# Optimization experiments

Hardware: AMD Instinct MI355X
Metric: run time of the kernel (lower is better)

## Reference

```python
import jax, jax.numpy as jnp
import numpy as np

N_NODES = 50000
N_EDGES = 800000
IN_CH = 128
OUT_CH = 64
HID_CH = 2 * OUT_CH  # 128


def gcn_conv(x, edge_index, W, b, n_nodes):
    """PyG GCNConv: linear -> add self-loops -> sym-normalized scatter-add -> bias."""
    h = x @ W  # [N, out]
    loop = jnp.arange(n_nodes)
    row = jnp.concatenate([edge_index[0], loop])  # source nodes
    col = jnp.concatenate([edge_index[1], loop])  # target nodes
    deg = jax.ops.segment_sum(jnp.ones_like(col, dtype=h.dtype), col, num_segments=n_nodes)
    dinv = jnp.where(deg > 0, jax.lax.rsqrt(jnp.maximum(deg, 1.0)), 0.0)
    norm = dinv[row] * dinv[col]  # [E+N]
    msg = h[row] * norm[:, None]  # gather + scale, [E+N, out]
    out = jax.ops.segment_sum(msg, col, num_segments=n_nodes)  # scatter-add
    return out + b


def setup_inputs() -> dict:
    key = jax.random.key(0)
    ks = jax.random.split(key, 9)
    x = jax.random.normal(ks[0], (N_NODES, IN_CH), dtype=jnp.float32)
    edge_index = jax.random.randint(ks[1], (2, N_EDGES), 0, N_NODES, dtype=jnp.int64)
    s_in = 1.0 / np.sqrt(IN_CH)
    s_hid = 1.0 / np.sqrt(HID_CH)
    W1 = jax.random.normal(ks[2], (IN_CH, HID_CH), dtype=jnp.float32) * s_in
    b1 = jnp.zeros((HID_CH,), dtype=jnp.float32)
    W2 = jax.random.normal(ks[3], (HID_CH, OUT_CH), dtype=jnp.float32) * s_hid
    b2 = jnp.zeros((OUT_CH,), dtype=jnp.float32)
    W3 = jax.random.normal(ks[4], (HID_CH, OUT_CH), dtype=jnp.float32) * s_hid
    b3 = jnp.zeros((OUT_CH,), dtype=jnp.float32)
    return {"x": x, "edge_index": edge_index, "W1": W1, "b1": b1,
            "W2": W2, "b2": b2, "W3": W3, "b3": b3}


def reference(x, edge_index, W1, b1, W2, b2, W3, b3):
    act = jax.nn.relu
    hidden = act(gcn_conv(x, edge_index, W1, b1, N_NODES))
    x1 = act(gcn_conv(hidden, edge_index, W2, b2, N_NODES))
    x2 = act(gcn_conv(hidden, edge_index, W3, b3, N_NODES))
    return (x1, x2)
```

## Files before the change

### kernel.cpp

```cpp
#include <hip/hip_runtime.h>

#define N_NODES 50000
#define N_EDGES 800000
#define CH 128
#define WT_PAD 136
#define DUMMY N_NODES
#define SLOT_LOG 6
#define AGG_HALF_BLKS 1563
#define PREP_THREADS (128 * 256)

typedef __attribute__((ext_vector_type(8))) short short8;
typedef __attribute__((ext_vector_type(4))) float floatx4;

__device__ __forceinline__ short f2bf(float f) {
    union { float f; unsigned u; } v; v.f = f;
    unsigned r = v.u + 0x7fff + ((v.u >> 16) & 1);
    return (short)(r >> 16);
}
__device__ __forceinline__ float bflo(unsigned u) {
    union { unsigned u; float f; } v; v.u = u << 16; return v.f;
}
__device__ __forceinline__ float bfhi(unsigned u) {
    union { unsigned u; float f; } v; v.u = u & 0xffff0000u; return v.f;
}


__global__ __launch_bounds__(256) void prep_kernel(const float* __restrict__ W1,
                                                   const float* __restrict__ W2,
                                                   const float* __restrict__ W3,
                                                   const float* __restrict__ b2,
                                                   const float* __restrict__ b3,
                                                   unsigned short* __restrict__ Wt1,
                                                   unsigned short* __restrict__ Wt23,
                                                   float* __restrict__ b23,
                                                   int* __restrict__ counts,
                                                   unsigned short* __restrict__ sorted_src,
                                                   unsigned int* __restrict__ gdummy) {
    int i = blockIdx.x * blockDim.x + threadIdx.x;
    if (i < 128 * 128) {
        int n = i >> 7, k = i & 127;
        Wt1[i] = (unsigned short)f2bf(W1[k * 128 + n]);
        float w = (n < 64) ? W2[k * 64 + n] : W3[k * 64 + (n - 64)];
        Wt23[i] = (unsigned short)f2bf(w);
    } else if (i < 128 * 128 + 128) {
        int k2 = i - 128 * 128;
        b23[k2] = (k2 < 64) ? b2[k2] : b3[k2 - 64];
    } else if (i < 128 * 128 + 192) {
        gdummy[i - (128 * 128 + 128)] = 0;
    }
    for (int j = i; j < N_NODES; j += PREP_THREADS) counts[j] = 0;
    const unsigned dpat = ((unsigned)DUMMY) | (((unsigned)DUMMY) << 16);
    uint4 dfill = make_uint4(dpat, dpat, dpat, dpat);
    uint4* sp = (uint4*)sorted_src;
    for (int j = i; j < (N_NODES << SLOT_LOG) / 8; j += PREP_THREADS) sp[j] = dfill;
}


__global__ void rank_scatter(const int* __restrict__ ei, int* __restrict__ counts,
                             unsigned short* __restrict__ sorted_src) {
    int e = blockIdx.x * blockDim.x + threadIdx.x;
    if (e < N_EDGES) {
        int src = __builtin_nontemporal_load(ei + e);
        int dst = __builtin_nontemporal_load(ei + N_EDGES + e);
        int r = atomicAdd(&counts[dst], 1);
        if (r < 64) sorted_src[(dst << SLOT_LOG) + r] = (unsigned short)src;
    }
}


template <bool A_BF16>
__global__ __launch_bounds__(256) void gemm_mfma(const void* __restrict__ Ain,
                                                 const unsigned short* __restrict__ Wt,
                                                 const int* __restrict__ degs,
                                                 unsigned short* __restrict__ g) {
    __shared__ unsigned short lds[128 * WT_PAD];
    int tid = threadIdx.x;
    int wave = tid >> 6, lane = tid & 63;
    int quad = lane >> 4, ln = lane & 15;

    {
        int r = tid >> 1, h = tid & 1;
        const int4* src = (const int4*)(Wt + r * 128 + h * 64);
#pragma unroll
        for (int i = 0; i < 8; ++i)
            *(int4*)&lds[r * WT_PAD + h * 64 + i * 8] = src[i];
    }

    int row_base = blockIdx.x * 64 + wave * 16;
    int arow = row_base + ln;
    bool ok = arow < N_NODES;
    short8 afrag[4];
    if (A_BF16) {
        const unsigned short* A = (const unsigned short*)Ain;
#pragma unroll
        for (int kk = 0; kk < 4; ++kk) {
            short8 v = {};
            if (ok) v = *(const short8*)(A + arow * 128 + kk * 32 + quad * 8);
            afrag[kk] = v;
        }
    } else {
        const float* A = (const float*)Ain;
#pragma unroll
        for (int kk = 0; kk < 4; ++kk) {
            short8 v = {};
            if (ok) {
                const floatx4* p = (const floatx4*)(A + arow * 128 + kk * 32 + quad * 8);
                floatx4 fa = p[0], fb = p[1];
                v[0] = f2bf(fa.x); v[1] = f2bf(fa.y); v[2] = f2bf(fa.z); v[3] = f2bf(fa.w);
                v[4] = f2bf(fb.x); v[5] = f2bf(fb.y); v[6] = f2bf(fb.z); v[7] = f2bf(fb.w);
            }
            afrag[kk] = v;
        }
    }
    __syncthreads();

    floatx4 acc[8] = {};
#pragma unroll
    for (int n0 = 0; n0 < 8; ++n0) {
#pragma unroll
        for (int kk = 0; kk < 4; ++kk) {
            short8 b = *(const short8*)&lds[(n0 * 16 + ln) * WT_PAD + kk * 32 + quad * 8];
            acc[n0] = __builtin_amdgcn_mfma_f32_16x16x32_bf16(afrag[kk], b, acc[n0], 0, 0, 0);
        }
    }

    __syncthreads();
    unsigned short* st = &lds[wave * 16 * WT_PAD];
    float dv[4];
#pragma unroll
    for (int r = 0; r < 4; ++r) {
        int node = row_base + quad * 4 + r;
        dv[r] = (node < N_NODES) ? rsqrtf((float)(degs[node] + 1)) : 0.f;
    }
#pragma unroll
    for (int n0 = 0; n0 < 8; ++n0)
#pragma unroll
        for (int r = 0; r < 4; ++r)
            st[(quad * 4 + r) * WT_PAD + n0 * 16 + ln] =
                (unsigned short)f2bf(acc[n0][r] * dv[r]);
    __syncthreads();

#pragma unroll
    for (int i = 0; i < 4; ++i) {
        int row = i * 4 + quad;
        int node = row_base + row;
        short8 v = *(const short8*)&st[row * WT_PAD + ln * 8];
        if (node < N_NODES) *(short8*)(g + node * 128 + ln * 8) = v;
    }
}


template <int MODE>
__global__ __launch_bounds__(256) void aggregate_bf16(const unsigned short* __restrict__ g,
                                                      const int* __restrict__ degs,
                                                      const unsigned short* __restrict__ srcs,
                                                      const float* __restrict__ bias,
                                                      void* __restrict__ outp) {
    int h = 0, nb = blockIdx.x;
    if (nb >= AGG_HALF_BLKS) { h = 1; nb -= AGG_HALF_BLKS; }
    int n = nb * 32 + (threadIdx.x >> 3);
    if (n >= N_NODES) return;
    int c4 = threadIdx.x & 7;
    int hoff = h * 8;
    const uint4* grow = (const uint4*)g;
    uint4 u = grow[n * 16 + hoff + c4];
    float a0 = bflo(u.x), a1 = bfhi(u.x), a2 = bflo(u.y), a3 = bfhi(u.y);
    float a4 = bflo(u.z), a5 = bfhi(u.z), a6 = bflo(u.w), a7 = bfhi(u.w);
    float c0 = 0.f, c1 = 0.f, c2 = 0.f, c3 = 0.f, c5 = 0.f, c6 = 0.f, c7 = 0.f, c8 = 0.f;
    int deg = degs[n];
    int beg = n << SLOT_LOG;
    int pend = beg + ((deg + 3) & ~3);
    int e = beg;
    for (; e + 8 <= pend; e += 8) {
        ushort4 sa = *(const ushort4*)&srcs[e];
        ushort4 sb = *(const ushort4*)&srcs[e + 4];
        uint4 v0 = grow[sa.x * 16 + hoff + c4];
        uint4 v1 = grow[sa.y * 16 + hoff + c4];
        uint4 v2 = grow[sa.z * 16 + hoff + c4];
        uint4 v3 = grow[sa.w * 16 + hoff + c4];
        uint4 v4 = grow[sb.x * 16 + hoff + c4];
        uint4 v5 = grow[sb.y * 16 + hoff + c4];
        uint4 v6 = grow[sb.z * 16 + hoff + c4];
        uint4 v7 = grow[sb.w * 16 + hoff + c4];
        a0 += bflo(v0.x); a1 += bfhi(v0.x); a2 += bflo(v0.y); a3 += bfhi(v0.y);
        a4 += bflo(v0.z); a5 += bfhi(v0.z); a6 += bflo(v0.w); a7 += bfhi(v0.w);
        c0 += bflo(v1.x); c1 += bfhi(v1.x); c2 += bflo(v1.y); c3 += bfhi(v1.y);
        c5 += bflo(v1.z); c6 += bfhi(v1.z); c7 += bflo(v1.w); c8 += bfhi(v1.w);
        a0 += bflo(v2.x); a1 += bfhi(v2.x); a2 += bflo(v2.y); a3 += bfhi(v2.y);
        a4 += bflo(v2.z); a5 += bfhi(v2.z); a6 += bflo(v2.w); a7 += bfhi(v2.w);
        c0 += bflo(v3.x); c1 += bfhi(v3.x); c2 += bflo(v3.y); c3 += bfhi(v3.y);
        c5 += bflo(v3.z); c6 += bfhi(v3.z); c7 += bflo(v3.w); c8 += bfhi(v3.w);
        a0 += bflo(v4.x); a1 += bfhi(v4.x); a2 += bflo(v4.y); a3 += bfhi(v4.y);
        a4 += bflo(v4.z); a5 += bfhi(v4.z); a6 += bflo(v4.w); a7 += bfhi(v4.w);
        c0 += bflo(v5.x); c1 += bfhi(v5.x); c2 += bflo(v5.y); c3 += bfhi(v5.y);
        c5 += bflo(v5.z); c6 += bfhi(v5.z); c7 += bflo(v5.w); c8 += bfhi(v5.w);
        a0 += bflo(v6.x); a1 += bfhi(v6.x); a2 += bflo(v6.y); a3 += bfhi(v6.y);
        a4 += bflo(v6.z); a5 += bfhi(v6.z); a6 += bflo(v6.w); a7 += bfhi(v6.w);
        c0 += bflo(v7.x); c1 += bfhi(v7.x); c2 += bflo(v7.y); c3 += bfhi(v7.y);
        c5 += bflo(v7.z); c6 += bfhi(v7.z); c7 += bflo(v7.w); c8 += bfhi(v7.w);
    }
    if (e < pend) {
        ushort4 sa = *(const ushort4*)&srcs[e];
        uint4 v0 = grow[sa.x * 16 + hoff + c4];
        uint4 v1 = grow[sa.y * 16 + hoff + c4];
        uint4 v2 = grow[sa.z * 16 + hoff + c4];
        uint4 v3 = grow[sa.w * 16 + hoff + c4];
        a0 += bflo(v0.x); a1 += bfhi(v0.x); a2 += bflo(v0.y); a3 += bfhi(v0.y);
        a4 += bflo(v0.z); a5 += bfhi(v0.z); a6 += bflo(v0.w); a7 += bfhi(v0.w);
        c0 += bflo(v1.x); c1 += bfhi(v1.x); c2 += bflo(v1.y); c3 += bfhi(v1.y);
        c5 += bflo(v1.z); c6 += bfhi(v1.z); c7 += bflo(v1.w); c8 += bfhi(v1.w);
        a0 += bflo(v2.x); a1 += bfhi(v2.x); a2 += bflo(v2.y); a3 += bfhi(v2.y);
        a4 += bflo(v2.z); a5 += bfhi(v2.z); a6 += bflo(v2.w); a7 += bfhi(v2.w);
        c0 += bflo(v3.x); c1 += bfhi(v3.x); c2 += bflo(v3.y); c3 += bfhi(v3.y);
        c5 += bflo(v3.z); c6 += bfhi(v3.z); c7 += bflo(v3.w); c8 += bfhi(v3.w);
    }
    a0 += c0; a1 += c1; a2 += c2; a3 += c3; a4 += c5; a5 += c6; a6 += c7; a7 += c8;
    float d = rsqrtf((float)(deg + 1));
    float4 bv0 = ((const float4*)bias)[h * 16 + c4 * 2];
    float4 bv1 = ((const float4*)bias)[h * 16 + c4 * 2 + 1];
    float o0 = fmaxf(d * a0 + bv0.x, 0.f);
    float o1 = fmaxf(d * a1 + bv0.y, 0.f);
    float o2 = fmaxf(d * a2 + bv0.z, 0.f);
    float o3 = fmaxf(d * a3 + bv0.w, 0.f);
    float o4 = fmaxf(d * a4 + bv1.x, 0.f);
    float o5 = fmaxf(d * a5 + bv1.y, 0.f);
    float o6 = fmaxf(d * a6 + bv1.z, 0.f);
    float o7 = fmaxf(d * a7 + bv1.w, 0.f);
    if (MODE == 0) {
        uint4 w;
        w.x = ((unsigned)(unsigned short)f2bf(o0)) | (((unsigned)(unsigned short)f2bf(o1)) << 16);
        w.y = ((unsigned)(unsigned short)f2bf(o2)) | (((unsigned)(unsigned short)f2bf(o3)) << 16);
        w.z = ((unsigned)(unsigned short)f2bf(o4)) | (((unsigned)(unsigned short)f2bf(o5)) << 16);
        w.w = ((unsigned)(unsigned short)f2bf(o6)) | (((unsigned)(unsigned short)f2bf(o7)) << 16);
        ((uint4*)outp)[n * 16 + hoff + c4] = w;
    } else {
        float* out = (float*)outp + (size_t)h * N_NODES * 64;
        floatx4* o = (floatx4*)out + n * 16 + c4 * 2;
        floatx4 w0; w0.x = o0; w0.y = o1; w0.z = o2; w0.w = o3;
        floatx4 w1; w1.x = o4; w1.y = o5; w1.z = o6; w1.w = o7;
        __builtin_nontemporal_store(w0, o);
        __builtin_nontemporal_store(w1, o + 1);
    }
}


extern "C" void kernel_launch(void* const* d_in, const int* in_sizes, int n_in,
                              void* d_out, int out_size, void* d_ws, size_t ws_size,
                              hipStream_t stream) {
    const float* x  = (const float*)d_in[0];
    const int*   ei = (const int*)d_in[1];
    const float* W1 = (const float*)d_in[2];
    const float* b1 = (const float*)d_in[3];
    const float* W2 = (const float*)d_in[4];
    const float* b2 = (const float*)d_in[5];
    const float* W3 = (const float*)d_in[6];
    const float* b3 = (const float*)d_in[7];
    float* out = (float*)d_out;

    char* w = (char*)d_ws;
    int*            counts     = (int*)(w + 0);
    unsigned short* sorted_src = (unsigned short*)(w + 3686400);
    unsigned short* Wt1        = (unsigned short*)(w + 10485760);
    unsigned short* Wt23       = (unsigned short*)(w + 10518528);
    float*          b23        = (float*)(w + 10551296);
    unsigned short* g1         = (unsigned short*)(w + 12582912);
    unsigned short* hidden     = (unsigned short*)(w + 25690112);

    prep_kernel<<<128, 256, 0, stream>>>(W1, W2, W3, b2, b3, Wt1, Wt23, b23, counts,
                                         sorted_src, (unsigned int*)(g1 + N_NODES * 128));
    rank_scatter<<<(N_EDGES + 255) / 256, 256, 0, stream>>>(ei, counts, sorted_src);

    const int gemm_blocks = (N_NODES + 63) / 64;
    const int agg_blocks = 2 * AGG_HALF_BLKS;

    gemm_mfma<false><<<gemm_blocks, 256, 0, stream>>>(x, Wt1, counts, g1);
    aggregate_bf16<0><<<agg_blocks, 256, 0, stream>>>(g1, counts, sorted_src, b1, hidden);

    gemm_mfma<true><<<gemm_blocks, 256, 0, stream>>>(hidden, Wt23, counts, g1);
    aggregate_bf16<1><<<agg_blocks, 256, 0, stream>>>(g1, counts, sorted_src, b23, out);
}
```

Before: 209.3 us.

## Replace global atomic edge scatter with two-pass bucketed partition and LDS CSR build

Graph preprocessing is rebuilt. Edges are first bucketed by destination into groups of 128 nodes using block-local histograms and scans, then each bucket builds its fixed-slot adjacency in shared memory and writes it out with coalesced stores. This replaces per-edge global atomics on node counters, scattered 2-byte global writes, and the full global dummy-fill of sorted_src. In exchange it adds one extra kernel and an intermediate buffer, buckets are capped at 3072 edges, and the aggregation now clamps degree to 64.

```diff
diff --git a/kernel.cpp b/kernel.cpp
--- a/kernel.cpp
+++ b/kernel.cpp
@@ -7,7 +7,11 @@
 #define DUMMY N_NODES
 #define SLOT_LOG 6
 #define AGG_HALF_BLKS 1563
-#define PREP_THREADS (128 * 256)
+
+#define NBUCK 391
+#define BUCK_CAP 3072
+#define EPB 4096
+#define PART_BLOCKS 196
 
 typedef __attribute__((ext_vector_type(8))) short short8;
 typedef __attribute__((ext_vector_type(4))) float floatx4;
@@ -33,8 +37,7 @@
                                                    unsigned short* __restrict__ Wt1,
                                                    unsigned short* __restrict__ Wt23,
                                                    float* __restrict__ b23,
-                                                   int* __restrict__ counts,
-                                                   unsigned short* __restrict__ sorted_src,
+                                                   int* __restrict__ bucket_cnt,
                                                    unsigned int* __restrict__ gdummy) {
     int i = blockIdx.x * blockDim.x + threadIdx.x;
     if (i < 128 * 128) {
@@ -48,22 +51,95 @@
     } else if (i < 128 * 128 + 192) {
         gdummy[i - (128 * 128 + 128)] = 0;
     }
-    for (int j = i; j < N_NODES; j += PREP_THREADS) counts[j] = 0;
+    if (i < NBUCK) bucket_cnt[i] = 0;
+}
+
+
+__global__ __launch_bounds__(256) void partition(const int* __restrict__ ei,
+                                                 int* __restrict__ bucket_cnt,
+                                                 unsigned* __restrict__ bucket_data) {
+    __shared__ int hcnt[512], hscan[512], htmp[512];
+    __shared__ int s_shift[512];
+    __shared__ unsigned stg[EPB];
+    __shared__ int dsti[EPB];
+    int tid = threadIdx.x;
+    int e0 = blockIdx.x * EPB;
+
+    for (int i = tid; i < 512; i += 256) hcnt[i] = 0;
+    __syncthreads();
+    for (int j = tid; j < EPB; j += 256) {
+        int e = e0 + j;
+        if (e < N_EDGES) atomicAdd(&hcnt[ei[N_EDGES + e] >> 7], 1);
+    }
+    __syncthreads();
+    for (int i = tid; i < 512; i += 256) hscan[i] = hcnt[i];
+    __syncthreads();
+    for (int off = 1; off < 512; off <<= 1) {
+        for (int i = tid; i < 512; i += 256) htmp[i] = hscan[i] + (i >= off ? hscan[i - off] : 0);
+        __syncthreads();
+        for (int i = tid; i < 512; i += 256) hscan[i] = htmp[i];
+        __syncthreads();
+    }
+    for (int b = tid; b < NBUCK; b += 256) {
+        int c = hcnt[b];
+        int excl = hscan[b] - c;
+        int g = (c > 0) ? atomicAdd(&bucket_cnt[b], c) : 0;
+        s_shift[b] = g - excl;
+        htmp[b] = excl;
+    }
+    __syncthreads();
+    for (int j = tid; j < EPB; j += 256) {
+        int e = e0 + j;
+        if (e < N_EDGES) {
+            int src = ei[e];
+            int d = ei[N_EDGES + e];
+            int b = d >> 7;
+            int pos = atomicAdd(&htmp[b], 1);
+            stg[pos] = ((unsigned)(d & 127) << 16) | (unsigned)src;
+            int gidx = s_shift[b] + pos;
+            dsti[pos] = (gidx < BUCK_CAP) ? (b * BUCK_CAP + gidx) : -1;
+        }
+    }
+    __syncthreads();
+    int tot = N_EDGES - e0; if (tot > EPB) tot = EPB;
+    for (int j = tid; j < tot; j += 256) {
+        int di = dsti[j];
+        if (di >= 0) bucket_data[di] = stg[j];
+    }
+}
+
+
+__global__ __launch_bounds__(256) void csr_build(const unsigned* __restrict__ bucket_data,
+                                                 const int* __restrict__ bucket_cnt,
+                                                 int* __restrict__ counts,
+                                                 unsigned short* __restrict__ sorted_src) {
+    __shared__ uint4 slots4[1024];
+    __shared__ int ctr[128];
+    unsigned short* slots = (unsigned short*)slots4;
+    int tid = threadIdx.x, b = blockIdx.x;
+
+    for (int i = tid; i < 128; i += 256) ctr[i] = 0;
     const unsigned dpat = ((unsigned)DUMMY) | (((unsigned)DUMMY) << 16);
-    uint4 dfill = make_uint4(dpat, dpat, dpat, dpat);
-    uint4* sp = (uint4*)sorted_src;
-    for (int j = i; j < (N_NODES << SLOT_LOG) / 8; j += PREP_THREADS) sp[j] = dfill;
-}
-
-
-__global__ void rank_scatter(const int* __restrict__ ei, int* __restrict__ counts,
-                             unsigned short* __restrict__ sorted_src) {
-    int e = blockIdx.x * blockDim.x + threadIdx.x;
-    if (e < N_EDGES) {
-        int src = __builtin_nontemporal_load(ei + e);
-        int dst = __builtin_nontemporal_load(ei + N_EDGES + e);
-        int r = atomicAdd(&counts[dst], 1);
-        if (r < 64) sorted_src[(dst << SLOT_LOG) + r] = (unsigned short)src;
+    for (int i = tid; i < 1024; i += 256) slots4[i] = make_uint4(dpat, dpat, dpat, dpat);
+    __syncthreads();
+
+    int cnt = bucket_cnt[b]; if (cnt > BUCK_CAP) cnt = BUCK_CAP;
+    const unsigned* bd = bucket_data + b * BUCK_CAP;
+    for (int j = tid; j < cnt; j += 256) {
+        unsigned w = bd[j];
+        int dl = (int)(w >> 16);
+        int r = atomicAdd(&ctr[dl], 1);
+        if (r < 64) slots[(dl << 6) + r] = (unsigned short)(w & 0xffffu);
+    }
+    __syncthreads();
+
+    int node0 = b << 7;
+    for (int i = tid; i < 128; i += 256)
+        if (node0 + i < N_NODES) counts[node0 + i] = ctr[i];
+    uint4* gs = (uint4*)(sorted_src + ((size_t)node0 << SLOT_LOG));
+    for (int k = tid; k < 1024; k += 256) {
+        int row = k >> 3;
+        if (node0 + row < N_NODES) gs[k] = slots4[k];
     }
 }
 
@@ -168,8 +244,9 @@
     float a4 = bflo(u.z), a5 = bfhi(u.z), a6 = bflo(u.w), a7 = bfhi(u.w);
     float c0 = 0.f, c1 = 0.f, c2 = 0.f, c3 = 0.f, c5 = 0.f, c6 = 0.f, c7 = 0.f, c8 = 0.f;
     int deg = degs[n];
+    int degc = deg > 64 ? 64 : deg;
     int beg = n << SLOT_LOG;
-    int pend = beg + ((deg + 3) & ~3);
+    int pend = beg + ((degc + 3) & ~3);
     int e = beg;
     for (; e + 8 <= pend; e += 8) {
         ushort4 sa = *(const ushort4*)&srcs[e];
@@ -258,17 +335,20 @@
     float* out = (float*)d_out;
 
     char* w = (char*)d_ws;
-    int*            counts     = (int*)(w + 0);
-    unsigned short* sorted_src = (unsigned short*)(w + 3686400);
-    unsigned short* Wt1        = (unsigned short*)(w + 10485760);
-    unsigned short* Wt23       = (unsigned short*)(w + 10518528);
-    float*          b23        = (float*)(w + 10551296);
-    unsigned short* g1         = (unsigned short*)(w + 12582912);
-    unsigned short* hidden     = (unsigned short*)(w + 25690112);
-
-    prep_kernel<<<128, 256, 0, stream>>>(W1, W2, W3, b2, b3, Wt1, Wt23, b23, counts,
-                                         sorted_src, (unsigned int*)(g1 + N_NODES * 128));
-    rank_scatter<<<(N_EDGES + 255) / 256, 256, 0, stream>>>(ei, counts, sorted_src);
+    int*            counts      = (int*)(w + 0);
+    int*            bucket_cnt  = (int*)(w + 200704);
+    unsigned short* Wt1         = (unsigned short*)(w + 204800);
+    unsigned short* Wt23        = (unsigned short*)(w + 237568);
+    float*          b23         = (float*)(w + 270336);
+    unsigned*       bucket_data = (unsigned*)(w + 278528);
+    unsigned short* sorted_src  = (unsigned short*)(w + 5083136);
+    unsigned short* g1          = (unsigned short*)(w + 11483136);
+    unsigned short* hidden      = (unsigned short*)(w + 24283392);
+
+    prep_kernel<<<66, 256, 0, stream>>>(W1, W2, W3, b2, b3, Wt1, Wt23, b23, bucket_cnt,
+                                        (unsigned int*)(g1 + N_NODES * 128));
+    partition<<<PART_BLOCKS, 256, 0, stream>>>(ei, bucket_cnt, bucket_data);
+    csr_build<<<NBUCK, 256, 0, stream>>>(bucket_data, bucket_cnt, counts, sorted_src);
 
     const int gemm_blocks = (N_NODES + 63) / 64;
     const int agg_blocks = 2 * AGG_HALF_BLKS;
```

Result: faster. 190.9 us (-8.8%).
